# Kernel optimization log

Measured on AMD Instinct MI355X. Metric: run time of the kernel, lower is better.

The kernel has to match this reference:

```python
import jax, jax.numpy as jnp
import numpy as np

B, C, T = 64, 384, 512
DUR_MAX = 8            # durations drawn from [0, 8)
MAX_NEW_TIME = 4096    # static padded output length >= T * (DUR_MAX - 1)


def setup_inputs() -> dict:
    key = jax.random.key(0)
    kx, kd = jax.random.split(key)
    x = jax.random.normal(kx, (B, C, T), dtype=jnp.float32)
    duration = jax.random.randint(kd, (B, 1, T), 0, DUR_MAX, dtype=jnp.int32)
    return {"x": x, "duration": duration}


def reference(x, duration):
    # x: [B, C, T] float32, duration: [B, 1, T] int32
    dur = duration[:, 0, :]                      # [B, T]
    csum = jnp.cumsum(dur, axis=-1)              # [B, T] exclusive-right cumsum boundaries
    total = csum[:, -1]                          # [B] expanded length per sample
    j = jnp.arange(MAX_NEW_TIME, dtype=jnp.int32)  # output frame positions
    # source phoneme index for each output frame: smallest t with j < csum[t]
    idx = jax.vmap(lambda c: jnp.searchsorted(c, j, side="right"))(csum)  # [B, MAX_NEW_TIME]
    idx = jnp.clip(idx, 0, T - 1)
    # gather along time, broadcast over channels -> [B, C, MAX_NEW_TIME]
    out = jnp.take_along_axis(x, idx[:, None, :].astype(jnp.int32), axis=-1)
    valid = j[None, :] < total[:, None]          # [B, MAX_NEW_TIME]
    out = jnp.where(valid[:, None, :], out, jnp.zeros((), dtype=x.dtype))
    # mask derived from non-zero values of channel 0, matching torch code
    new_mask = (out[:, 0:1, :] != 0).astype(jnp.int32)  # [B, 1, MAX_NEW_TIME]
    return out, new_mask
```

## Files before the change

### kernel.cpp

```cpp
#include <hip/hip_runtime.h>


#define BB 64
#define CC 384
#define TT 512
#define TOUT 4096
#define CB 16

__global__ __launch_bounds__(TT) void build_idx_kernel(
    const int* __restrict__ dur, int* __restrict__ idx) {
  const int b = blockIdx.x;
  const int t = threadIdx.x;

  __shared__ int s[TT];
  const int d = dur[b * TT + t];
  s[t] = d;
  __syncthreads();

  for (int off = 1; off < TT; off <<= 1) {
    int v = (t >= off) ? s[t - off] : 0;
    __syncthreads();
    s[t] += v;
    __syncthreads();
  }

  const int end = s[t];
  const int start = end - d;

  int* __restrict__ idxb = idx + b * TOUT;
  #pragma unroll
  for (int k = 0; k < TOUT / TT; ++k) idxb[t + k * TT] = -1;
  __syncthreads();

  for (int p = start; p < end; ++p) idxb[p] = t;
}

__global__ __launch_bounds__(256) void gather_kernel(
    const float* __restrict__ x, const int* __restrict__ idx,
    float* __restrict__ out, float* __restrict__ mask) {
  const int b = blockIdx.y;
  const int c0 = blockIdx.x * CB;
  const int tid = threadIdx.x;

  __shared__ float xs[CB * TT];

  const float4* __restrict__ xb4 =
      (const float4*)(x + ((size_t)b * CC + c0) * TT);
  float4* __restrict__ xs4 = (float4*)xs;
  #pragma unroll
  for (int k = 0; k < (CB * TT / 4) / 256; ++k)
    xs4[k * 256 + tid] = xb4[k * 256 + tid];

  const int4* __restrict__ ib4 = (const int4*)(idx + (size_t)b * TOUT);
  int4 I[TOUT / 1024];
  #pragma unroll
  for (int jt = 0; jt < TOUT / 1024; ++jt)
    I[jt] = ib4[jt * 256 + tid];

  __syncthreads();

  float* __restrict__ ob = out + ((size_t)b * CC + c0) * TOUT + tid * 4;

  #pragma unroll
  for (int c = 0; c < CB; ++c) {
    const float* __restrict__ xr = xs + c * TT;
    #pragma unroll
    for (int jt = 0; jt < TOUT / 1024; ++jt) {
      const int4 i4 = I[jt];
      float4 v;
      v.x = (i4.x >= 0) ? xr[i4.x] : 0.0f;
      v.y = (i4.y >= 0) ? xr[i4.y] : 0.0f;
      v.z = (i4.z >= 0) ? xr[i4.z] : 0.0f;
      v.w = (i4.w >= 0) ? xr[i4.w] : 0.0f;
      *(float4*)(ob + (size_t)c * TOUT + jt * 1024) = v;

      if (c == 0 && c0 == 0) {
        float4 m;
        m.x = (v.x != 0.0f) ? 1.0f : 0.0f;
        m.y = (v.y != 0.0f) ? 1.0f : 0.0f;
        m.z = (v.z != 0.0f) ? 1.0f : 0.0f;
        m.w = (v.w != 0.0f) ? 1.0f : 0.0f;
        *(float4*)(mask + (size_t)b * TOUT + jt * 1024 + tid * 4) = m;
      }
    }
  }
}

extern "C" void kernel_launch(void* const* d_in, const int* in_sizes, int n_in,
                              void* d_out, int out_size, void* d_ws, size_t ws_size,
                              hipStream_t stream) {
  const float* x = (const float*)d_in[0];
  const int* dur = (const int*)d_in[1];

  float* out = (float*)d_out;
  float* mask = out + (size_t)BB * CC * TOUT;

  int* idx = (int*)d_ws;

  build_idx_kernel<<<BB, TT, 0, stream>>>(dur, idx);
  gather_kernel<<<dim3(CC / CB, BB), 256, 0, stream>>>(x, idx, out, mask);
}
```

Before: 432.8 us.

## Fuse index construction into gather kernel using LDS scan per block

Drops the separate index-building kernel and its global workspace. Each gather block now recomputes the duration prefix sum (two durations per thread) and the index map in shared memory, reusing the x tile buffer, while the x tile is held in registers until the map is done. The output loop order is swapped to iterate channels innermost per index chunk. This removes one launch and a global round-trip, at the cost of repeating the scan in every channel block and higher register pressure.

```diff
diff --git a/kernel.cpp b/kernel.cpp
--- a/kernel.cpp
+++ b/kernel.cpp
@@ -7,71 +7,70 @@
 #define TOUT 4096
 #define CB 16
 
-__global__ __launch_bounds__(TT) void build_idx_kernel(
-    const int* __restrict__ dur, int* __restrict__ idx) {
-  const int b = blockIdx.x;
-  const int t = threadIdx.x;
-
-  __shared__ int s[TT];
-  const int d = dur[b * TT + t];
-  s[t] = d;
-  __syncthreads();
-
-  for (int off = 1; off < TT; off <<= 1) {
-    int v = (t >= off) ? s[t - off] : 0;
-    __syncthreads();
-    s[t] += v;
-    __syncthreads();
-  }
-
-  const int end = s[t];
-  const int start = end - d;
-
-  int* __restrict__ idxb = idx + b * TOUT;
-  #pragma unroll
-  for (int k = 0; k < TOUT / TT; ++k) idxb[t + k * TT] = -1;
-  __syncthreads();
-
-  for (int p = start; p < end; ++p) idxb[p] = t;
-}
-
-__global__ __launch_bounds__(256) void gather_kernel(
-    const float* __restrict__ x, const int* __restrict__ idx,
+__global__ __launch_bounds__(256) void length_regulator_fused(
+    const float* __restrict__ x, const int* __restrict__ dur,
     float* __restrict__ out, float* __restrict__ mask) {
   const int b = blockIdx.y;
   const int c0 = blockIdx.x * CB;
   const int tid = threadIdx.x;
 
   __shared__ float xs[CB * TT];
+  int* const idx_lds = (int*)xs;
+  int* const spair   = (int*)xs + TOUT;
 
   const float4* __restrict__ xb4 =
       (const float4*)(x + ((size_t)b * CC + c0) * TT);
-  float4* __restrict__ xs4 = (float4*)xs;
+  float4 xr[CB * TT / 4 / 256];
   #pragma unroll
-  for (int k = 0; k < (CB * TT / 4) / 256; ++k)
-    xs4[k * 256 + tid] = xb4[k * 256 + tid];
+  for (int k = 0; k < CB * TT / 4 / 256; ++k)
+    xr[k] = xb4[k * 256 + tid];
 
-  const int4* __restrict__ ib4 = (const int4*)(idx + (size_t)b * TOUT);
+  const int2 d2 = ((const int2*)(dur + (size_t)b * TT))[tid];
+  spair[tid] = d2.x + d2.y;
+  #pragma unroll
+  for (int k = 0; k < TOUT / 256; ++k) idx_lds[k * 256 + tid] = -1;
+  __syncthreads();
+
+  #pragma unroll
+  for (int off = 1; off < 256; off <<= 1) {
+    const int v = (tid >= off) ? spair[tid - off] : 0;
+    __syncthreads();
+    spair[tid] += v;
+    __syncthreads();
+  }
+
+  const int e1 = spair[tid];
+  const int s1 = e1 - d2.y;
+  const int s0 = s1 - d2.x;
+  for (int p = s0; p < s1; ++p) idx_lds[p] = 2 * tid;
+  for (int p = s1; p < e1; ++p) idx_lds[p] = 2 * tid + 1;
+  __syncthreads();
+
   int4 I[TOUT / 1024];
   #pragma unroll
   for (int jt = 0; jt < TOUT / 1024; ++jt)
-    I[jt] = ib4[jt * 256 + tid];
+    I[jt] = ((const int4*)idx_lds)[jt * 256 + tid];
+  __syncthreads();
 
+  float4* const xs4 = (float4*)xs;
+  #pragma unroll
+  for (int k = 0; k < CB * TT / 4 / 256; ++k)
+    xs4[k * 256 + tid] = xr[k];
   __syncthreads();
 
   float* __restrict__ ob = out + ((size_t)b * CC + c0) * TOUT + tid * 4;
 
   #pragma unroll
-  for (int c = 0; c < CB; ++c) {
-    const float* __restrict__ xr = xs + c * TT;
+  for (int jt = 0; jt < TOUT / 1024; ++jt) {
+    const int4 i4 = I[jt];
     #pragma unroll
-    for (int jt = 0; jt < TOUT / 1024; ++jt) {
-      const int4 i4 = I[jt];
+    for (int c = 0; c < CB; ++c) {
+      const float* __restrict__ row = xs + c * TT;
       float4 v;
-      v.x = (i4.x >= 0) ? xr[i4.x] : 0.0f;
-      v.y = (i4.y >= 0) ? xr[i4.y] : 0.0f;
-      v.z = (i4.z >= 0) ? xr[i4.z] : 0.0f;
-      v.w = (i4.w >= 0) ? xr[i4.w] : 0.0f;
+      v.x = (i4.x >= 0) ? row[i4.x] : 0.0f;
+      v.y = (i4.y >= 0) ? row[i4.y] : 0.0f;
+      v.z = (i4.z >= 0) ? row[i4.z] : 0.0f;
+      v.w = (i4.w >= 0) ? row[i4.w] : 0.0f;
       *(float4*)(ob + (size_t)c * TOUT + jt * 1024) = v;
 
       if (c == 0 && c0 == 0) {
@@ -95,8 +94,5 @@
   float* out = (float*)d_out;
   float* mask = out + (size_t)BB * CC * TOUT;
 
-  int* idx = (int*)d_ws;
-
-  build_idx_kernel<<<BB, TT, 0, stream>>>(dur, idx);
-  gather_kernel<<<dim3(CC / CB, BB), 256, 0, stream>>>(x, idx, out, mask);
+  length_regulator_fused<<<dim3(CC / CB, BB), 256, 0, stream>>>(x, dur, out, mask);
 }
```

Result: no change. 437.0 us (+1.0%).
